# Optimization experiments

Hardware: AMD Instinct MI355X
Metric: run time of the kernel (lower is better)

Reference implementation:

```python
import jax, jax.numpy as jnp
import numpy as np

B, S, D = 4, 2048, 1024
NEG = -1e10

def setup_inputs() -> dict:
    key = jax.random.key(0)
    ks = jax.random.split(key, 10)
    inv = 1.0 / np.sqrt(D)
    return {
        "Q": jax.random.normal(ks[0], (B, S, D), dtype=jnp.float32),
        "K": jax.random.normal(ks[1], (B, S, D), dtype=jnp.float32),
        "V": jax.random.normal(ks[2], (B, S, D), dtype=jnp.float32),
        "attention_mask": jax.random.randint(ks[3], (B, 1, S), 0, 2, dtype=jnp.int32),
        "Wq": jax.random.uniform(ks[4], (D, D), jnp.float32, -inv, inv),
        "bq": jnp.zeros((D,), jnp.float32),
        "Wk": jax.random.uniform(ks[5], (D, D), jnp.float32, -inv, inv),
        "bk": jnp.zeros((D,), jnp.float32),
        "Wv": jax.random.uniform(ks[6], (D, D), jnp.float32, -inv, inv),
        "bv": jnp.zeros((D,), jnp.float32),
    }

def reference(Q, K, V, attention_mask, Wq, bq, Wk, bk, Wv, bv):
    # QKV projections (dropout is identity in eval mode)
    q = jnp.einsum('bsd,ed->bse', Q, Wq) + bq  # [B,S,D]
    k = jnp.einsum('bsd,ed->bse', K, Wk) + bk
    v = jnp.einsum('bsd,ed->bse', V, Wv) + bv
    scores = jnp.einsum('bqd,bkd->bqk', q, k) / jnp.sqrt(jnp.float32(D))  # [B,S,S]
    scores = jnp.where(attention_mask == 0, jnp.float32(NEG), scores)
    # additive causal mask: upper triangle (diag=1) gets NEG
    causal = jnp.triu(jnp.full((S, S), NEG, dtype=jnp.float32), k=1)
    scores = scores + causal
    attn = jax.nn.softmax(scores, axis=-1)
    return jnp.einsum('bqk,bkd->bqd', attn, v)
```

## Files before the change

kernel.cpp:

```cpp
#include <hip/hip_runtime.h>
#include <hip/hip_bf16.h>

typedef __bf16 bf16x8 __attribute__((ext_vector_type(8)));
typedef float floatx4 __attribute__((ext_vector_type(4)));
typedef unsigned short ushort_t;

__device__ __forceinline__ bf16x8 load8f(const float* p) {
  const float4* q = reinterpret_cast<const float4*>(p);
  float4 x = q[0], y = q[1];
  bf16x8 r;
  r[0] = (__bf16)x.x; r[1] = (__bf16)x.y; r[2] = (__bf16)x.z; r[3] = (__bf16)x.w;
  r[4] = (__bf16)y.x; r[5] = (__bf16)y.y; r[6] = (__bf16)y.z; r[7] = (__bf16)y.w;
  return r;
}

__device__ __forceinline__ void storeC(float* C, long idx, float v) { C[idx] = v; }
__device__ __forceinline__ void storeC(ushort_t* C, long idx, float v) {
  __bf16 b = (__bf16)v;
  C[idx] = __builtin_bit_cast(ushort_t, b);
}

__device__ __forceinline__ void glds16(const ushort_t* g, ushort_t* l) {
  __builtin_amdgcn_global_load_lds(
      (const __attribute__((address_space(1))) void*)g,
      (__attribute__((address_space(3))) void*)l, 16, 0, 0);
}

__global__ __launch_bounds__(256) void f32_to_bf16(
    const float* __restrict__ src, ushort_t* __restrict__ dst, long n)
{
  const long i = (((long)blockIdx.x * 256) + threadIdx.x) * 8;
  if (i < n) {
    bf16x8 v = load8f(src + i);
    *reinterpret_cast<bf16x8*>(dst + i) = v;
  }
}

template<typename TC, int BIAS_MODE>
__global__ __launch_bounds__(256) void gemm_nt_bf16(
    const ushort_t* __restrict__ A, const ushort_t* __restrict__ B,
    const float* __restrict__ bias, TC* __restrict__ C,
    int M, int N, int K, float alpha,
    long sAb, long sBb, long sCb)
{
  __shared__ ushort_t As[128 * 32];
  __shared__ ushort_t Bs[128 * 32];

  const int bz = blockIdx.z;
  A += (long)bz * sAb;
  B += (long)bz * sBb;
  C += (long)bz * sCb;

  const int bm = blockIdx.x, bn = blockIdx.y;
  const int tid = threadIdx.x;
  const int wave = tid >> 6, lane = tid & 63;
  const int wm = (wave & 1) * 64, wn = (wave >> 1) * 64;
  const int lr = lane & 15, lq = lane >> 4;

  const ushort_t* Ab = A + (long)(bm * 128) * K;
  const ushort_t* Bb = B + (long)(bn * 128) * K;

  const int seg0 = tid, seg1 = 256 + tid;
  const int sr0 = seg0 >> 2, sk0 = (seg0 & 3) << 3;
  const int sr1 = seg1 >> 2, sk1 = (seg1 & 3) << 3;

  floatx4 acc[4][4];
  #pragma unroll
  for (int i = 0; i < 4; ++i)
    #pragma unroll
    for (int j = 0; j < 4; ++j)
      acc[i][j] = (floatx4){0.f, 0.f, 0.f, 0.f};

  int aoff[4], boff[4];
  #pragma unroll
  for (int i = 0; i < 4; ++i) {
    aoff[i] = (wm + i * 16 + lr) * 32 + lq * 8;
    boff[i] = (wn + i * 16 + lr) * 32 + lq * 8;
  }

  const int ktiles = K >> 5;
  for (int kt = 0; kt < ktiles; ++kt) {
    const int kc = kt << 5;
    glds16(Ab + (long)sr0 * K + kc + sk0, &As[seg0 * 8]);
    glds16(Ab + (long)sr1 * K + kc + sk1, &As[seg1 * 8]);
    glds16(Bb + (long)sr0 * K + kc + sk0, &Bs[seg0 * 8]);
    glds16(Bb + (long)sr1 * K + kc + sk1, &Bs[seg1 * 8]);
    __syncthreads();

    bf16x8 af[4], bfr[4];
    #pragma unroll
    for (int i = 0; i < 4; ++i)
      af[i] = *reinterpret_cast<const bf16x8*>(&As[aoff[i]]);
    #pragma unroll
    for (int j = 0; j < 4; ++j)
      bfr[j] = *reinterpret_cast<const bf16x8*>(&Bs[boff[j]]);
    #pragma unroll
    for (int i = 0; i < 4; ++i)
      #pragma unroll
      for (int j = 0; j < 4; ++j)
        acc[i][j] = __builtin_amdgcn_mfma_f32_16x16x32_bf16(af[i], bfr[j], acc[i][j], 0, 0, 0);
    __syncthreads();
  }

  #pragma unroll
  for (int i = 0; i < 4; ++i) {
    #pragma unroll
    for (int j = 0; j < 4; ++j) {
      const int row0 = bm * 128 + wm + i * 16 + lq * 4;
      const int col  = bn * 128 + wn + j * 16 + lr;
      #pragma unroll
      for (int r = 0; r < 4; ++r) {
        float v = acc[i][j][r] * alpha;
        if (BIAS_MODE == 1) v += bias[col];
        if (BIAS_MODE == 2) v += bias[row0 + r];
        storeC(C, (long)(row0 + r) * N + col, v);
      }
    }
  }
}

__global__ __launch_bounds__(256) void softmax_causal(
    const float* __restrict__ Sc, ushort_t* __restrict__ P,
    const int* __restrict__ mask, int S)
{
  const int i = blockIdx.x, b = blockIdx.y;
  const float* row = Sc + ((long)b * S + i) * S;
  ushort_t* prow = P + ((long)b * S + i) * S;
  const int* mrow = mask + (long)b * S;
  const int tid = threadIdx.x;
  const int lane = tid & 63, wave = tid >> 6;
  __shared__ float red[4];

  float vals[8];
  float mymax = -3.4e38f;
  #pragma unroll
  for (int u = 0; u < 8; ++u) {
    const int j = tid + (u << 8);
    float v = row[j];
    if (mrow[j] == 0) v = -1e10f;
    if (j > i) v += -1e10f;
    vals[u] = v;
    mymax = fmaxf(mymax, v);
  }
  #pragma unroll
  for (int off = 32; off; off >>= 1)
    mymax = fmaxf(mymax, __shfl_xor(mymax, off));
  if (lane == 0) red[wave] = mymax;
  __syncthreads();
  const float m = fmaxf(fmaxf(red[0], red[1]), fmaxf(red[2], red[3]));
  __syncthreads();

  float sum = 0.f;
  #pragma unroll
  for (int u = 0; u < 8; ++u) {
    const float e = __expf(vals[u] - m);
    vals[u] = e;
    sum += e;
  }
  #pragma unroll
  for (int off = 32; off; off >>= 1)
    sum += __shfl_xor(sum, off);
  if (lane == 0) red[wave] = sum;
  __syncthreads();
  const float tot = red[0] + red[1] + red[2] + red[3];
  const float inv = 1.0f / tot;
  #pragma unroll
  for (int u = 0; u < 8; ++u) {
    const int j = tid + (u << 8);
    __bf16 bv = (__bf16)(vals[u] * inv);
    prow[j] = __builtin_bit_cast(ushort_t, bv);
  }
}

extern "C" void kernel_launch(void* const* d_in, const int* in_sizes, int n_in,
                              void* d_out, int out_size, void* d_ws, size_t ws_size,
                              hipStream_t stream)
{
  const int B = 4, S = 2048, D = 1024;
  const float* Q  = (const float*)d_in[0];
  const float* K  = (const float*)d_in[1];
  const float* V  = (const float*)d_in[2];
  const int*   am = (const int*)d_in[3];
  const float* Wq = (const float*)d_in[4];
  const float* bq = (const float*)d_in[5];
  const float* Wk = (const float*)d_in[6];
  const float* bk = (const float*)d_in[7];
  const float* Wv = (const float*)d_in[8];
  const float* bv = (const float*)d_in[9];
  float* out = (float*)d_out;

  const long MS = (long)B * S;
  const long NQ = MS * D;
  const long NW = (long)D * D;

  ushort_t* qb = (ushort_t*)d_ws;
  ushort_t* kb = qb + NQ;
  ushort_t* vT = kb + NQ;
  float*    Sc = (float*)(vT + NQ);
  ushort_t* P  = qb;

  ushort_t* Qb  = (ushort_t*)Sc;
  ushort_t* Kb  = Qb + NQ;
  ushort_t* Vb  = Kb + NQ;
  ushort_t* Wqb = Vb + NQ;
  ushort_t* Wkb = Wqb + NW;
  ushort_t* Wvb = Wkb + NW;

  dim3 blk(256);

  f32_to_bf16<<<dim3((int)(NQ / 2048)), blk, 0, stream>>>(Q, Qb, NQ);
  f32_to_bf16<<<dim3((int)(NQ / 2048)), blk, 0, stream>>>(K, Kb, NQ);
  f32_to_bf16<<<dim3((int)(NQ / 2048)), blk, 0, stream>>>(V, Vb, NQ);
  f32_to_bf16<<<dim3((int)(NW / 2048)), blk, 0, stream>>>(Wq, Wqb, NW);
  f32_to_bf16<<<dim3((int)(NW / 2048)), blk, 0, stream>>>(Wk, Wkb, NW);
  f32_to_bf16<<<dim3((int)(NW / 2048)), blk, 0, stream>>>(Wv, Wvb, NW);

  gemm_nt_bf16<ushort_t, 1><<<dim3(64, 8, 1), blk, 0, stream>>>(
      Qb, Wqb, bq, qb, (int)MS, D, D, 1.0f, 0L, 0L, 0L);
  gemm_nt_bf16<ushort_t, 1><<<dim3(64, 8, 1), blk, 0, stream>>>(
      Kb, Wkb, bk, kb, (int)MS, D, D, 1.0f, 0L, 0L, 0L);
  gemm_nt_bf16<ushort_t, 2><<<dim3(8, 16, 4), blk, 0, stream>>>(
      Wvb, Vb, bv, vT, D, S, D, 1.0f, 0L, (long)S * D, (long)D * S);

  gemm_nt_bf16<float, 0><<<dim3(16, 16, 4), blk, 0, stream>>>(
      qb, kb, nullptr, Sc, S, S, D, 0.03125f,
      (long)S * D, (long)S * D, (long)S * S);
  softmax_causal<<<dim3(S, B), blk, 0, stream>>>(Sc, P, am, S);
  gemm_nt_bf16<float, 0><<<dim3(16, 8, 4), blk, 0, stream>>>(
      P, vT, nullptr, out, S, D, S, 1.0f,
      (long)S * S, (long)D * S, (long)S * D);
}
```

Measured before the change: 386.1 us.

## Batch conversions, store scores in bf16, skip causally masked score tiles

Merges the six f32-to-bf16 conversion launches into two batched launches and the Q/K projections into one batched GEMM. The score matrix is now written as bf16 instead of fp32, which halves its write and read traffic, and softmax reads and writes with vectorized 8-wide accesses. A new kernel finds the first unmasked key per batch so that score tiles strictly above the diagonal can be skipped when the mask guarantees they are dropped. The skipped tiles are left uninitialized and softmax still reads them, which is only safe if those values are always overridden. Rounding scores to bf16 before softmax costs some accuracy.

New measurement: 376.5 us. 2.5% less time.

```diff
diff --git a/kernel.cpp b/kernel.cpp
--- a/kernel.cpp
+++ b/kernel.cpp
@@ -26,32 +26,61 @@
       (__attribute__((address_space(3))) void*)l, 16, 0, 0);
 }
 
-__global__ __launch_bounds__(256) void f32_to_bf16(
-    const float* __restrict__ src, ushort_t* __restrict__ dst, long n)
-{
+__global__ __launch_bounds__(256) void cvt3(
+    const float* __restrict__ s0, const float* __restrict__ s1,
+    const float* __restrict__ s2, ushort_t* __restrict__ dst, long n)
+{
+  const int z = blockIdx.y;
+  const float* s = (z == 0) ? s0 : ((z == 1) ? s1 : s2);
+  ushort_t* d = dst + (long)z * n;
   const long i = (((long)blockIdx.x * 256) + threadIdx.x) * 8;
   if (i < n) {
-    bf16x8 v = load8f(src + i);
-    *reinterpret_cast<bf16x8*>(dst + i) = v;
-  }
-}
-
-template<typename TC, int BIAS_MODE>
+    bf16x8 v = load8f(s + i);
+    *reinterpret_cast<bf16x8*>(d + i) = v;
+  }
+}
+
+__global__ __launch_bounds__(256) void find_j0(
+    const int* __restrict__ mask, int* __restrict__ j0, int S)
+{
+  const int b = blockIdx.x;
+  const int* m = mask + (long)b * S;
+  const int tid = threadIdx.x;
+  int best = S;
+  for (int j = tid; j < S; j += 256)
+    if (m[j] != 0) best = min(best, j);
+  #pragma unroll
+  for (int off = 32; off; off >>= 1)
+    best = min(best, __shfl_xor(best, off));
+  __shared__ int red[4];
+  if ((tid & 63) == 0) red[tid >> 6] = best;
+  __syncthreads();
+  if (tid == 0) j0[b] = min(min(red[0], red[1]), min(red[2], red[3]));
+}
+
+template<typename TC, int BIAS_MODE, bool CSKIP>
 __global__ __launch_bounds__(256) void gemm_nt_bf16(
     const ushort_t* __restrict__ A, const ushort_t* __restrict__ B,
-    const float* __restrict__ bias, TC* __restrict__ C,
+    const float* __restrict__ bias, const float* __restrict__ bias_b,
+    TC* __restrict__ C, const int* __restrict__ j0p,
     int M, int N, int K, float alpha,
     long sAb, long sBb, long sCb)
 {
+  const int bz = blockIdx.z;
+  const int bm = blockIdx.x, bn = blockIdx.y;
+
+  if (CSKIP) {
+    if (bn > bm && j0p[bz] <= bm * 128) return;
+  }
+
   __shared__ ushort_t As[128 * 32];
   __shared__ ushort_t Bs[128 * 32];
 
-  const int bz = blockIdx.z;
   A += (long)bz * sAb;
   B += (long)bz * sBb;
   C += (long)bz * sCb;
-
-  const int bm = blockIdx.x, bn = blockIdx.y;
+  if (BIAS_MODE == 1 && bz == 1 && bias_b) bias = bias_b;
+
   const int tid = threadIdx.x;
   const int wave = tid >> 6, lane = tid & 63;
   const int wm = (wave & 1) * 64, wn = (wave >> 1) * 64;
@@ -120,24 +149,30 @@
 }
 
 __global__ __launch_bounds__(256) void softmax_causal(
-    const float* __restrict__ Sc, ushort_t* __restrict__ P,
+    const ushort_t* __restrict__ Sc, ushort_t* __restrict__ P,
     const int* __restrict__ mask, int S)
 {
   const int i = blockIdx.x, b = blockIdx.y;
-  const float* row = Sc + ((long)b * S + i) * S;
+  const ushort_t* row = Sc + ((long)b * S + i) * S;
   ushort_t* prow = P + ((long)b * S + i) * S;
   const int* mrow = mask + (long)b * S;
   const int tid = threadIdx.x;
   const int lane = tid & 63, wave = tid >> 6;
+  const int j0 = tid * 8;
   __shared__ float red[4];
+
+  bf16x8 sv = *reinterpret_cast<const bf16x8*>(row + j0);
+  const int4* mp = reinterpret_cast<const int4*>(mrow + j0);
+  int4 m0 = mp[0], m1 = mp[1];
+  int mk[8] = {m0.x, m0.y, m0.z, m0.w, m1.x, m1.y, m1.z, m1.w};
 
   float vals[8];
   float mymax = -3.4e38f;
   #pragma unroll
   for (int u = 0; u < 8; ++u) {
-    const int j = tid + (u << 8);
-    float v = row[j];
-    if (mrow[j] == 0) v = -1e10f;
+    const int j = j0 + u;
+    float v = (float)sv[u];
+    if (mk[u] == 0) v = -1e10f;
     if (j > i) v += -1e10f;
     vals[u] = v;
     mymax = fmaxf(mymax, v);
@@ -164,12 +199,11 @@
   __syncthreads();
   const float tot = red[0] + red[1] + red[2] + red[3];
   const float inv = 1.0f / tot;
-  #pragma unroll
-  for (int u = 0; u < 8; ++u) {
-    const int j = tid + (u << 8);
-    __bf16 bv = (__bf16)(vals[u] * inv);
-    prow[j] = __builtin_bit_cast(ushort_t, bv);
-  }
+
+  bf16x8 pv;
+  #pragma unroll
+  for (int u = 0; u < 8; ++u) pv[u] = (__bf16)(vals[u] * inv);
+  *reinterpret_cast<bf16x8*>(prow + j0) = pv;
 }
 
 extern "C" void kernel_launch(void* const* d_in, const int* in_sizes, int n_in,
@@ -192,41 +226,34 @@
   const long MS = (long)B * S;
   const long NQ = MS * D;
   const long NW = (long)D * D;
+  const long NS = (long)B * S * S;
 
   ushort_t* qb = (ushort_t*)d_ws;
   ushort_t* kb = qb + NQ;
   ushort_t* vT = kb + NQ;
-  float*    Sc = (float*)(vT + NQ);
+  ushort_t* Qb = vT + NQ;
+  ushort_t* Wqb = Qb + 3 * NQ;
+  int* j0 = (int*)(Wqb + 3 * NW);
+  ushort_t* Sc = Qb;
   ushort_t* P  = qb;
 
-  ushort_t* Qb  = (ushort_t*)Sc;
-  ushort_t* Kb  = Qb + NQ;
-  ushort_t* Vb  = Kb + NQ;
-  ushort_t* Wqb = Vb + NQ;
-  ushort_t* Wkb = Wqb + NW;
-  ushort_t* Wvb = Wkb + NW;
-
   dim3 blk(256);
 
-  f32_to_bf16<<<dim3((int)(NQ / 2048)), blk, 0, stream>>>(Q, Qb, NQ);
-  f32_to_bf16<<<dim3((int)(NQ / 2048)), blk, 0, stream>>>(K, Kb, NQ);
-  f32_to_bf16<<<dim3((int)(NQ / 2048)), blk, 0, stream>>>(V, Vb, NQ);
-  f32_to_bf16<<<dim3((int)(NW / 2048)), blk, 0, stream>>>(Wq, Wqb, NW);
-  f32_to_bf16<<<dim3((int)(NW / 2048)), blk, 0, stream>>>(Wk, Wkb, NW);
-  f32_to_bf16<<<dim3((int)(NW / 2048)), blk, 0, stream>>>(Wv, Wvb, NW);
-
-  gemm_nt_bf16<ushort_t, 1><<<dim3(64, 8, 1), blk, 0, stream>>>(
-      Qb, Wqb, bq, qb, (int)MS, D, D, 1.0f, 0L, 0L, 0L);
-  gemm_nt_bf16<ushort_t, 1><<<dim3(64, 8, 1), blk, 0, stream>>>(
-      Kb, Wkb, bk, kb, (int)MS, D, D, 1.0f, 0L, 0L, 0L);
-  gemm_nt_bf16<ushort_t, 2><<<dim3(8, 16, 4), blk, 0, stream>>>(
-      Wvb, Vb, bv, vT, D, S, D, 1.0f, 0L, (long)S * D, (long)D * S);
-
-  gemm_nt_bf16<float, 0><<<dim3(16, 16, 4), blk, 0, stream>>>(
-      qb, kb, nullptr, Sc, S, S, D, 0.03125f,
+  cvt3<<<dim3((int)(NQ / 2048), 3), blk, 0, stream>>>(Q, K, V, Qb, NQ);
+  cvt3<<<dim3((int)(NW / 2048), 3), blk, 0, stream>>>(Wq, Wk, Wv, Wqb, NW);
+  find_j0<<<dim3(B), blk, 0, stream>>>(am, j0, S);
+
+  gemm_nt_bf16<ushort_t, 1, false><<<dim3(64, 8, 2), blk, 0, stream>>>(
+      Qb, Wqb, bq, bk, qb, nullptr, (int)MS, D, D, 1.0f, NQ, NW, NQ);
+  gemm_nt_bf16<ushort_t, 2, false><<<dim3(8, 16, 4), blk, 0, stream>>>(
+      Wqb + 2 * NW, Qb + 2 * NQ, bv, nullptr, vT, nullptr,
+      D, S, D, 1.0f, 0L, (long)S * D, (long)D * S);
+
+  gemm_nt_bf16<ushort_t, 0, true><<<dim3(16, 16, 4), blk, 0, stream>>>(
+      qb, kb, nullptr, nullptr, Sc, j0, S, S, D, 0.03125f,
       (long)S * D, (long)S * D, (long)S * S);
   softmax_causal<<<dim3(S, B), blk, 0, stream>>>(Sc, P, am, S);
-  gemm_nt_bf16<float, 0><<<dim3(16, 8, 4), blk, 0, stream>>>(
-      P, vT, nullptr, out, S, D, S, 1.0f,
+  gemm_nt_bf16<float, 0, false><<<dim3(16, 8, 4), blk, 0, stream>>>(
+      P, vT, nullptr, nullptr, out, nullptr, S, D, S, 1.0f,
       (long)S * S, (long)D * S, (long)S * D);
 }
```
